# Optimization experiments

Measured on AMD Instinct MI355X. Metric: run time of the kernel, lower is better.

## Reference

```python
import jax, jax.numpy as jnp
import numpy as np

N_AP, N_UE, D = 256, 1024, 64  # dimension = 64 in source

def setup_inputs() -> dict:
    key = jax.random.key(0)
    ks = jax.random.split(key, 9)
    s = 1.0 / np.sqrt(2 * D)
    return {
        "ap_hid": jax.random.normal(ks[0], (N_AP, D), jnp.float32),
        "ue_hid": jax.random.normal(ks[1], (N_UE, D), jnp.float32),
        "edge_hid": jax.random.normal(ks[2], (N_AP, N_UE, D), jnp.float32),
        "W1": jax.random.normal(ks[3], (2 * D, D), jnp.float32) * s,
        "b1": jnp.zeros((D,), jnp.float32),
        "W2": jax.random.normal(ks[4], (2 * D, D), jnp.float32) * s,
        "b2": jnp.zeros((D,), jnp.float32),
        "W3": jax.random.normal(ks[5], (2 * D, D), jnp.float32) * s,
        "b3": jnp.zeros((D,), jnp.float32),
    }

def reference(ap_hid, ue_hid, edge_hid, W1, b1, W2, b2, W3, b3):
    # edge_hid[a, u] is the feature of edge (AP a, UE u); eid is (a, u) itself.
    A, U, d = edge_hid.shape

    # reduce_func_ap: per-AP mailbox over all UE neighbors -> mlp1(cat(ap_hid, edge_hid))
    ap_in = jnp.concatenate(
        [jnp.broadcast_to(ap_hid[:, None, :], (A, U, d)), edge_hid], axis=-1)  # [A,U,2d]
    ap_res = jax.nn.relu(jnp.einsum('auk,kd->aud', ap_in, W1) + b1)            # [A,U,d]

    # reduce_func_ue: per-UE mailbox over all AP neighbors -> mlp2(cat(ue_hid, edge_hid))
    edge_ua = jnp.swapaxes(edge_hid, 0, 1)                                     # [U,A,d]
    ue_in = jnp.concatenate(
        [jnp.broadcast_to(ue_hid[:, None, :], (U, A, d)), edge_ua], axis=-1)   # [U,A,2d]
    ue_res = jax.nn.relu(jnp.einsum('uak,kd->uad', ue_in, W2) + b2)            # [U,A,d]

    # message_func_edge: for edge (a,u), sum src AP's ap_result excluding the
    # mailbox slot whose eid matches this edge, plus same for dst UE's ue_result.
    ap_sum = ap_res.sum(axis=1)   # [A,d]
    ue_sum = ue_res.sum(axis=1)   # [U,d]
    agg = (ap_sum[:, None, :] - ap_res) \
        + (ue_sum[None, :, :] - jnp.swapaxes(ue_res, 0, 1))                     # [A,U,d]

    new = jnp.einsum('auk,kd->aud', jnp.concatenate([edge_hid, agg], axis=-1), W3) + b3
    return new  # new edge 'hid' for both AP2UE and UE2AP, shape [A,U,d]
```

## Files before the change

### kernel.cpp

```cpp
#include <hip/hip_runtime.h>


#define A_N 256
#define U_N 1024

typedef short short8 __attribute__((ext_vector_type(8)));
typedef float f32x4 __attribute__((ext_vector_type(4)));

__device__ __forceinline__ unsigned short f2bf(float f) {
  unsigned int u = __float_as_uint(f);
  return (unsigned short)((u + 0x7FFFu + ((u >> 16) & 1u)) >> 16);
}

__device__ __forceinline__ f32x4 mfma16(short8 a, short8 b, f32x4 c) {
  return __builtin_amdgcn_mfma_f32_16x16x32_bf16(a, b, c, 0, 0, 0);
}

__device__ __forceinline__ void cvt16(const float4& e0, const float4& e1,
                                      const float4& e2, const float4& e3,
                                      short8& a0, short8& a1) {
  a0[0] = (short)f2bf(e0.x); a0[1] = (short)f2bf(e0.y);
  a0[2] = (short)f2bf(e0.z); a0[3] = (short)f2bf(e0.w);
  a0[4] = (short)f2bf(e1.x); a0[5] = (short)f2bf(e1.y);
  a0[6] = (short)f2bf(e1.z); a0[7] = (short)f2bf(e1.w);
  a1[0] = (short)f2bf(e2.x); a1[1] = (short)f2bf(e2.y);
  a1[2] = (short)f2bf(e2.z); a1[3] = (short)f2bf(e2.w);
  a1[4] = (short)f2bf(e3.x); a1[5] = (short)f2bf(e3.y);
  a1[6] = (short)f2bf(e3.z); a1[7] = (short)f2bf(e3.w);
}

__device__ __forceinline__ void rowmlp_row(const float* __restrict__ in,
                                           const float* __restrict__ W,
                                           const float* __restrict__ bias,
                                           float* __restrict__ out, int r, int lane) {
  float rv = in[r * 64 + lane];
  float acc = bias ? bias[lane] : 0.f;
#pragma unroll
  for (int k = 0; k < 64; k++) acc += __shfl(rv, k, 64) * W[k * 64 + lane];
  out[r * 64 + lane] = acc;
}

__global__ __launch_bounds__(256) void k_prep(
    const float* __restrict__ ap_hid, const float* __restrict__ ue_hid,
    const float* __restrict__ W1, const float* __restrict__ b1,
    const float* __restrict__ W2, const float* __restrict__ b2,
    const float* __restrict__ W3, unsigned short* __restrict__ Wt,
    float* __restrict__ acc_zero, float* __restrict__ c1, float* __restrict__ c2) {
  int bx = blockIdx.x, tid = threadIdx.x;
  if (bx < 320) {
    int i = bx * 256 + tid;
    if (i < 81920) acc_zero[i] = 0.f;
  } else if (bx < 384) {
    int idx = (bx - 320) * 256 + tid;
    int r = idx >> 6, k = idx & 63;
    int sec = r >> 6, d = r & 63;
    float v;
    if (sec == 0)      v = W1[(64 + k) * 64 + d];
    else if (sec == 1) v = W2[(64 + k) * 64 + d];
    else if (sec == 2) v = W3[k * 64 + d];
    else               v = W3[(64 + k) * 64 + d];
    Wt[r * 64 + k] = f2bf(v);
  } else if (bx < 448) {
    int r = (bx - 384) * 4 + (tid >> 6);
    rowmlp_row(ap_hid, W1, b1, c1, r, tid & 63);
  } else {
    int r = (bx - 448) * 4 + (tid >> 6);
    rowmlp_row(ue_hid, W2, b2, c2, r, tid & 63);
  }
}

__global__ __launch_bounds__(256) void k_post(
    const float* __restrict__ ap_sum, const float* __restrict__ ue_sum,
    const float* __restrict__ W3, const float* __restrict__ b3,
    float* __restrict__ s3, float* __restrict__ s4) {
  int bx = blockIdx.x, tid = threadIdx.x;
  if (bx < 64) {
    int r = bx * 4 + (tid >> 6);
    rowmlp_row(ap_sum, W3 + 4096, nullptr, s3, r, tid & 63);
  } else {
    int r = (bx - 64) * 4 + (tid >> 6);
    rowmlp_row(ue_sum, W3 + 4096, b3, s4, r, tid & 63);
  }
}

__global__ __launch_bounds__(256) void k_pass1(
    const float* __restrict__ edge, const unsigned short* __restrict__ Wt,
    const float* __restrict__ c1, const float* __restrict__ c2,
    float* __restrict__ ap_sum, float* __restrict__ ue_sum) {
  int tid = threadIdx.x, lane = tid & 63, w = tid >> 6;
  int fr = lane & 15, fq = lane >> 4;
  int a0 = (blockIdx.x >> 4) * 4;
  int u0 = (blockIdx.x & 15) * 64;
  int urow = u0 + w * 16 + fr;
  const float* erow = edge + urow * 64 + fq * 8;

  short8 bw[8][2];
#pragma unroll
  for (int nt = 0; nt < 8; nt++)
#pragma unroll
    for (int ks = 0; ks < 2; ks++)
      bw[nt][ks] = *(const short8*)(Wt + (nt * 16 + fr) * 64 + ks * 32 + fq * 8);

  float c2v[4][4];
#pragma unroll
  for (int j = 0; j < 4; j++)
#pragma unroll
    for (int i = 0; i < 4; i++)
      c2v[j][i] = c2[(u0 + w * 16 + fq * 4 + i) * 64 + j * 16 + fr];

  float ureg[4][4];
#pragma unroll
  for (int j = 0; j < 4; j++)
#pragma unroll
    for (int i = 0; i < 4; i++) ureg[j][i] = 0.f;

  const float* p0 = erow + a0 * 65536;
  float4 e0 = *(const float4*)(p0);
  float4 e1 = *(const float4*)(p0 + 4);
  float4 e2 = *(const float4*)(p0 + 32);
  float4 e3 = *(const float4*)(p0 + 36);
  float c1v[4];
#pragma unroll
  for (int j = 0; j < 4; j++) c1v[j] = c1[a0 * 64 + j * 16 + fr];

  for (int c = 0; c < 4; c++) {
    int a = a0 + c;
    float4 n0, n1, n2, n3;
    float nc1[4];
    if (c < 3) {
      const float* np = erow + (a + 1) * 65536;
      n0 = *(const float4*)(np);
      n1 = *(const float4*)(np + 4);
      n2 = *(const float4*)(np + 32);
      n3 = *(const float4*)(np + 36);
#pragma unroll
      for (int j = 0; j < 4; j++) nc1[j] = c1[(a + 1) * 64 + j * 16 + fr];
    }
    short8 af0, af1;
    cvt16(e0, e1, e2, e3, af0, af1);

#pragma unroll
    for (int j = 0; j < 4; j++) {
      f32x4 acc = {0.f, 0.f, 0.f, 0.f};
      acc = mfma16(af0, bw[j][0], acc);
      acc = mfma16(af1, bw[j][1], acc);
      float cv = c1v[j];
      float rs = fmaxf(acc[0] + cv, 0.f) + fmaxf(acc[1] + cv, 0.f) +
                 fmaxf(acc[2] + cv, 0.f) + fmaxf(acc[3] + cv, 0.f);
      rs += __shfl_xor(rs, 16, 64);
      rs += __shfl_xor(rs, 32, 64);
      if (lane < 16) atomicAdd(&ap_sum[a * 64 + j * 16 + lane], rs);
    }
#pragma unroll
    for (int j = 0; j < 4; j++) {
      f32x4 acc = {0.f, 0.f, 0.f, 0.f};
      acc = mfma16(af0, bw[4 + j][0], acc);
      acc = mfma16(af1, bw[4 + j][1], acc);
#pragma unroll
      for (int i = 0; i < 4; i++)
        ureg[j][i] += fmaxf(acc[i] + c2v[j][i], 0.f);
    }
    if (c < 3) {
      e0 = n0; e1 = n1; e2 = n2; e3 = n3;
#pragma unroll
      for (int j = 0; j < 4; j++) c1v[j] = nc1[j];
    }
  }
#pragma unroll
  for (int j = 0; j < 4; j++)
#pragma unroll
    for (int i = 0; i < 4; i++)
      atomicAdd(&ue_sum[(u0 + w * 16 + fq * 4 + i) * 64 + j * 16 + fr], ureg[j][i]);
}

__global__ __launch_bounds__(256) void k_pass2(
    const float* __restrict__ edge, const unsigned short* __restrict__ Wt,
    const float* __restrict__ c1, const float* __restrict__ c2,
    const float* __restrict__ s3, const float* __restrict__ s4,
    float* __restrict__ out) {
  __shared__ unsigned short W_lds[256 * 72];
  __shared__ unsigned short t_lds[64 * 72];
  int tid = threadIdx.x, lane = tid & 63, w = tid >> 6;
  int fr = lane & 15, fq = lane >> 4;
  int a = blockIdx.x >> 2;
  int ubase = (blockIdx.x & 3) * 256;

#pragma unroll
  for (int it = 0; it < 8; it++) {
    int r = it * 32 + (tid >> 3), seg = tid & 7;
    *(uint4*)&W_lds[r * 72 + seg * 8] = *(const uint4*)(Wt + r * 64 + seg * 8);
  }

  float c1v[4], s3v[4];
#pragma unroll
  for (int j = 0; j < 4; j++) {
    c1v[j] = c1[a * 64 + j * 16 + fr];
    s3v[j] = s3[a * 64 + j * 16 + fr];
  }

  const float* er0 = edge + (a * 1024 + ubase + w * 16 + fr) * 64 + fq * 8;
  float4 e0 = *(const float4*)(er0);
  float4 e1 = *(const float4*)(er0 + 4);
  float4 e2 = *(const float4*)(er0 + 32);
  float4 e3 = *(const float4*)(er0 + 36);

  __syncthreads();

  for (int pnl = 0; pnl < 4; pnl++) {
    int upan = ubase + pnl * 64;
    float4 n0, n1, n2, n3;
    if (pnl < 3) {
      const float* nr = edge + (a * 1024 + upan + 64 + w * 16 + fr) * 64 + fq * 8;
      n0 = *(const float4*)(nr);
      n1 = *(const float4*)(nr + 4);
      n2 = *(const float4*)(nr + 32);
      n3 = *(const float4*)(nr + 36);
    }
    float c2v[4][4], s4v[4][4];
#pragma unroll
    for (int j = 0; j < 4; j++)
#pragma unroll
      for (int i = 0; i < 4; i++) {
        int u = upan + w * 16 + fq * 4 + i;
        c2v[j][i] = c2[u * 64 + j * 16 + fr];
        s4v[j][i] = s4[u * 64 + j * 16 + fr];
      }
    short8 af0, af1;
    cvt16(e0, e1, e2, e3, af0, af1);

    f32x4 accP3[4];
#pragma unroll
    for (int j = 0; j < 4; j++) {
      const unsigned short* wr = &W_lds[(j * 16 + fr) * 72 + fq * 8];
      short8 b10 = *(const short8*)(wr);
      short8 b11 = *(const short8*)(wr + 32);
      short8 b20 = *(const short8*)(wr + 64 * 72);
      short8 b21 = *(const short8*)(wr + 64 * 72 + 32);
      short8 b30 = *(const short8*)(wr + 128 * 72);
      short8 b31 = *(const short8*)(wr + 128 * 72 + 32);
      f32x4 a1 = {0.f, 0.f, 0.f, 0.f};
      a1 = mfma16(af0, b10, a1);
      a1 = mfma16(af1, b11, a1);
      f32x4 a2 = {0.f, 0.f, 0.f, 0.f};
      a2 = mfma16(af0, b20, a2);
      a2 = mfma16(af1, b21, a2);
      f32x4 p3 = {0.f, 0.f, 0.f, 0.f};
      p3 = mfma16(af0, b30, p3);
      p3 = mfma16(af1, b31, p3);
      accP3[j] = p3;
#pragma unroll
      for (int i = 0; i < 4; i++) {
        float tv = fmaxf(a1[i] + c1v[j], 0.f) + fmaxf(a2[i] + c2v[j][i], 0.f);
        t_lds[(w * 16 + fq * 4 + i) * 72 + j * 16 + fr] = f2bf(tv);
      }
    }
    short8 tf0 = *(const short8*)&t_lds[(w * 16 + fr) * 72 + fq * 8];
    short8 tf1 = *(const short8*)&t_lds[(w * 16 + fr) * 72 + 32 + fq * 8];
#pragma unroll
    for (int j = 0; j < 4; j++) {
      const unsigned short* wr = &W_lds[(192 + j * 16 + fr) * 72 + fq * 8];
      short8 b0 = *(const short8*)(wr);
      short8 b1 = *(const short8*)(wr + 32);
      f32x4 acc = {0.f, 0.f, 0.f, 0.f};
      acc = mfma16(tf0, b0, acc);
      acc = mfma16(tf1, b1, acc);
#pragma unroll
      for (int i = 0; i < 4; i++) {
        int u = upan + w * 16 + fq * 4 + i;
        out[(a * 1024 + u) * 64 + j * 16 + fr] =
            accP3[j][i] - acc[i] + s3v[j] + s4v[j][i];
      }
    }
    if (pnl < 3) { e0 = n0; e1 = n1; e2 = n2; e3 = n3; }
  }
}

extern "C" void kernel_launch(void* const* d_in, const int* in_sizes, int n_in,
                              void* d_out, int out_size, void* d_ws, size_t ws_size,
                              hipStream_t stream) {
  const float* ap_hid = (const float*)d_in[0];
  const float* ue_hid = (const float*)d_in[1];
  const float* edge   = (const float*)d_in[2];
  const float* W1     = (const float*)d_in[3];
  const float* b1     = (const float*)d_in[4];
  const float* W2     = (const float*)d_in[5];
  const float* b2     = (const float*)d_in[6];
  const float* W3     = (const float*)d_in[7];
  const float* b3     = (const float*)d_in[8];
  float* out = (float*)d_out;

  char* ws = (char*)d_ws;
  unsigned short* Wt = (unsigned short*)ws;
  float* c1     = (float*)(ws + 32768);
  float* c2     = (float*)(ws + 98304);
  float* ap_sum = (float*)(ws + 360448);
  float* ue_sum = (float*)(ws + 425984);
  float* s3     = (float*)(ws + 688128);
  float* s4     = (float*)(ws + 753664);

  k_prep<<<704, 256, 0, stream>>>(ap_hid, ue_hid, W1, b1, W2, b2, W3, Wt,
                                  (float*)(ws + 360448), c1, c2);
  k_pass1<<<1024, 256, 0, stream>>>(edge, Wt, c1, c2, ap_sum, ue_sum);
  k_post<<<320, 256, 0, stream>>>(ap_sum, ue_sum, W3, b3, s3, s4);
  k_pass2<<<1024, 256, 0, stream>>>(edge, Wt, c1, c2, s3, s4, out);
}
```

Measured before the change: 174.8 us.

## Replace global float atomics with per-block partial sums reduced in mid kernel

Per-AP sums now accumulate in shared memory via LDS atomics, and per-UE sums are written as plain stores into per-chunk partial buffers instead of global atomicAdd. A new mid kernel reduces the 16 AP partials and 64 UE partials before the W3 row transform, which also removes the zeroing pass from the prep kernel. This avoids contention and ordering cost from global atomics, but adds about 16 MB of partial-buffer writes and reads.

```diff
diff --git a/kernel.cpp b/kernel.cpp
--- a/kernel.cpp
+++ b/kernel.cpp
@@ -45,13 +45,10 @@
     const float* __restrict__ W1, const float* __restrict__ b1,
     const float* __restrict__ W2, const float* __restrict__ b2,
     const float* __restrict__ W3, unsigned short* __restrict__ Wt,
-    float* __restrict__ acc_zero, float* __restrict__ c1, float* __restrict__ c2) {
+    float* __restrict__ c1, float* __restrict__ c2) {
   int bx = blockIdx.x, tid = threadIdx.x;
-  if (bx < 320) {
-    int i = bx * 256 + tid;
-    if (i < 81920) acc_zero[i] = 0.f;
-  } else if (bx < 384) {
-    int idx = (bx - 320) * 256 + tid;
+  if (bx < 64) {
+    int idx = bx * 256 + tid;
     int r = idx >> 6, k = idx & 63;
     int sec = r >> 6, d = r & 63;
     float v;
@@ -60,39 +57,31 @@
     else if (sec == 2) v = W3[k * 64 + d];
     else               v = W3[(64 + k) * 64 + d];
     Wt[r * 64 + k] = f2bf(v);
-  } else if (bx < 448) {
-    int r = (bx - 384) * 4 + (tid >> 6);
+  } else if (bx < 128) {
+    int r = (bx - 64) * 4 + (tid >> 6);
     rowmlp_row(ap_hid, W1, b1, c1, r, tid & 63);
   } else {
-    int r = (bx - 448) * 4 + (tid >> 6);
+    int r = (bx - 128) * 4 + (tid >> 6);
     rowmlp_row(ue_hid, W2, b2, c2, r, tid & 63);
-  }
-}
-
-__global__ __launch_bounds__(256) void k_post(
-    const float* __restrict__ ap_sum, const float* __restrict__ ue_sum,
-    const float* __restrict__ W3, const float* __restrict__ b3,
-    float* __restrict__ s3, float* __restrict__ s4) {
-  int bx = blockIdx.x, tid = threadIdx.x;
-  if (bx < 64) {
-    int r = bx * 4 + (tid >> 6);
-    rowmlp_row(ap_sum, W3 + 4096, nullptr, s3, r, tid & 63);
-  } else {
-    int r = (bx - 64) * 4 + (tid >> 6);
-    rowmlp_row(ue_sum, W3 + 4096, b3, s4, r, tid & 63);
   }
 }
 
 __global__ __launch_bounds__(256) void k_pass1(
     const float* __restrict__ edge, const unsigned short* __restrict__ Wt,
     const float* __restrict__ c1, const float* __restrict__ c2,
-    float* __restrict__ ap_sum, float* __restrict__ ue_sum) {
+    float* __restrict__ ap_part, float* __restrict__ ue_part) {
+  __shared__ float ap_l[4 * 64];
   int tid = threadIdx.x, lane = tid & 63, w = tid >> 6;
   int fr = lane & 15, fq = lane >> 4;
-  int a0 = (blockIdx.x >> 4) * 4;
-  int u0 = (blockIdx.x & 15) * 64;
+  int chunk = blockIdx.x >> 4;
+  int panel = blockIdx.x & 15;
+  int a0 = chunk * 4;
+  int u0 = panel * 64;
   int urow = u0 + w * 16 + fr;
   const float* erow = edge + urow * 64 + fq * 8;
+
+  ap_l[tid] = 0.f;
+  __syncthreads();
 
   short8 bw[8][2];
 #pragma unroll
@@ -149,7 +138,7 @@
                  fmaxf(acc[2] + cv, 0.f) + fmaxf(acc[3] + cv, 0.f);
       rs += __shfl_xor(rs, 16, 64);
       rs += __shfl_xor(rs, 32, 64);
-      if (lane < 16) atomicAdd(&ap_sum[a * 64 + j * 16 + lane], rs);
+      if (lane < 16) atomicAdd(&ap_l[c * 64 + j * 16 + lane], rs);
     }
 #pragma unroll
     for (int j = 0; j < 4; j++) {
@@ -170,7 +159,37 @@
   for (int j = 0; j < 4; j++)
 #pragma unroll
     for (int i = 0; i < 4; i++)
-      atomicAdd(&ue_sum[(u0 + w * 16 + fq * 4 + i) * 64 + j * 16 + fr], ureg[j][i]);
+      ue_part[(chunk * 1024 + u0 + w * 16 + fq * 4 + i) * 64 + j * 16 + fr] =
+          ureg[j][i];
+  __syncthreads();
+  ap_part[(panel * 256 + a0 + w) * 64 + lane] = ap_l[tid];
+}
+
+__global__ __launch_bounds__(256) void k_mid(
+    const float* __restrict__ ap_part, const float* __restrict__ ue_part,
+    const float* __restrict__ W3, const float* __restrict__ b3,
+    float* __restrict__ s3, float* __restrict__ s4) {
+  int bx = blockIdx.x, tid = threadIdx.x, lane = tid & 63;
+  const float* W3b = W3 + 4096;
+  if (bx < 64) {
+    int r = bx * 4 + (tid >> 6);
+    float v = 0.f;
+#pragma unroll
+    for (int p = 0; p < 16; p++) v += ap_part[(p * 256 + r) * 64 + lane];
+    float acc = 0.f;
+#pragma unroll
+    for (int k = 0; k < 64; k++) acc += __shfl(v, k, 64) * W3b[k * 64 + lane];
+    s3[r * 64 + lane] = acc;
+  } else {
+    int r = (bx - 64) * 4 + (tid >> 6);
+    float v = 0.f;
+#pragma unroll
+    for (int p = 0; p < 64; p++) v += ue_part[(p * 1024 + r) * 64 + lane];
+    float acc = b3[lane];
+#pragma unroll
+    for (int k = 0; k < 64; k++) acc += __shfl(v, k, 64) * W3b[k * 64 + lane];
+    s4[r * 64 + lane] = acc;
+  }
 }
 
 __global__ __launch_bounds__(256) void k_pass2(
@@ -291,16 +310,15 @@
 
   char* ws = (char*)d_ws;
   unsigned short* Wt = (unsigned short*)ws;
-  float* c1     = (float*)(ws + 32768);
-  float* c2     = (float*)(ws + 98304);
-  float* ap_sum = (float*)(ws + 360448);
-  float* ue_sum = (float*)(ws + 425984);
-  float* s3     = (float*)(ws + 688128);
-  float* s4     = (float*)(ws + 753664);
-
-  k_prep<<<704, 256, 0, stream>>>(ap_hid, ue_hid, W1, b1, W2, b2, W3, Wt,
-                                  (float*)(ws + 360448), c1, c2);
-  k_pass1<<<1024, 256, 0, stream>>>(edge, Wt, c1, c2, ap_sum, ue_sum);
-  k_post<<<320, 256, 0, stream>>>(ap_sum, ue_sum, W3, b3, s3, s4);
+  float* c1      = (float*)(ws + 32768);
+  float* c2      = (float*)(ws + 98304);
+  float* s3      = (float*)(ws + 360448);
+  float* s4      = (float*)(ws + 425984);
+  float* ap_part = (float*)(ws + 688128);
+  float* ue_part = (float*)(ws + 4882432);
+
+  k_prep<<<384, 256, 0, stream>>>(ap_hid, ue_hid, W1, b1, W2, b2, W3, Wt, c1, c2);
+  k_pass1<<<1024, 256, 0, stream>>>(edge, Wt, c1, c2, ap_part, ue_part);
+  k_mid<<<320, 256, 0, stream>>>(ap_part, ue_part, W3, b3, s3, s4);
   k_pass2<<<1024, 256, 0, stream>>>(edge, Wt, c1, c2, s3, s4, out);
 }
```

New measurement: 171.2 us. -2.1%, faster.
